# Optimization experiments

Measured on AMD Instinct MI355X. Metric: run time of the kernel, lower is better.

## Reference

```python
import jax, jax.numpy as jnp
import numpy as np

SR = 4  # search_range
D = 2 * SR + 1  # 9
NC = D * D      # 81 output channels


def setup_inputs() -> dict:
    key = jax.random.key(0)
    k1, k2 = jax.random.split(key)
    B, C, H, W = 8, 64, 192, 256
    x1 = jax.random.normal(k1, (B, C, H, W), dtype=jnp.float32)
    x2 = jax.random.normal(k2, (B, C, H, W), dtype=jnp.float32)
    return {"x1": x1, "x2": x2}


def reference(x1, x2):
    B, C, H, W = x1.shape
    # Zero-pad x2 so out-of-overlap products are zero, matching the
    # zero-initialized cv in the original module.
    x2p = jnp.pad(x2, ((0, 0), (0, 0), (SR, SR), (SR, SR)))
    outs = [None] * NC
    for i in range(-SR, SR + 1):
        for j in range(-SR, SR + 1):
            # Original torch code uses cv[:, 9*i + j] with negative wraparound.
            k = (D * i + j) % NC
            # x2 sample position is (h - i, w - j); in padded coords start = SR - i.
            shifted = jax.lax.dynamic_slice(
                x2p, (0, 0, SR - i, SR - j), (B, C, H, W))
            outs[k] = jnp.sum(x1 * shifted, axis=1)  # [B, H, W]
    cv = jnp.stack(outs, axis=1)  # [B, 81, H, W]
    return cv / NC
```

## Files before the change

### kernel.cpp

```cpp
#include <hip/hip_runtime.h>

#define HH 192
#define WW 256
#define CCH 4
#define NCHUNK 16
#define THREADS 512
#define CHSTEP (CCH * HH * WW)
#define ROWF 264
#define CHF  (8 * ROWF)
#define BUFF (CCH * CHF)
#define NSTRIPS 33

typedef float f4 __attribute__((ext_vector_type(4)));

#define GLL(gp, lp) __builtin_amdgcn_global_load_lds(                        \
    (const __attribute__((address_space(1))) unsigned int*)(gp),            \
    (__attribute__((address_space(3))) unsigned int*)(lp), 16, 0, 0)

__global__ __launch_bounds__(THREADS) void cost_volume_kernel(
    const float* __restrict__ x1, const float* __restrict__ x2,
    float* __restrict__ out)
{
    __shared__ __align__(16) float smem[2 * BUFF];

    const int tid  = threadIdx.x;
    const int wave = tid >> 6;
    const int lane = tid & 63;

    const int bid = blockIdx.x;
    const bool isB = (bid >= 1536);
    int b, hout, hbase, drow;
    if (!isB) {
        b     = bid & 7;
        hout  = bid >> 3;
        hbase = hout - 3;
        drow  = 7 - wave;
    } else {
        const int t = bid - 1536;
        b     = t & 7;
        const int h0 = (t >> 3) << 3;
        hout  = h0 + wave;
        hbase = h0 - 4;
        drow  = wave;
    }

    auto desc = [&](int s, int& goff) {
        const int u = (s << 6) + lane;
        const int ch = u / 528, v = u % 528;
        const int d = v / 66, cu = v % 66;
        const int hg = hbase + d, wg = (cu << 2) - 4;
        const bool ok = (cu >= 1) & (cu <= 64) & (hg >= 0) & (hg < HH);
        goff = ok ? (((b * 64 + ch) * HH + hg) * WW + wg) : -1;
    };
    int g0, g1, g2, g3, g4;
    desc(wave,      g0);
    desc(wave + 8,  g1);
    desc(wave + 16, g2);
    desc(wave + 24, g3);
    desc(32,        g4);
    if (wave != 0) g4 = -1;

    auto issue = [&](int nb, int n) {
        const int cofs = n * CHSTEP;
        float* const base = smem + nb * BUFF;
        if (g0 >= 0) GLL(x2 + g0 + cofs, base + (wave << 8));
        if (g1 >= 0) GLL(x2 + g1 + cofs, base + ((wave + 8) << 8));
        if (g2 >= 0) GLL(x2 + g2 + cofs, base + ((wave + 16) << 8));
        if (g3 >= 0) GLL(x2 + g3 + cofs, base + ((wave + 24) << 8));
        if (g4 >= 0) GLL(x2 + g4 + cofs, base + (32 << 8));
    };

    const f4 z4 = {0.f, 0.f, 0.f, 0.f};
    for (int z = tid; z < 2 * BUFF / 4; z += THREADS) ((f4*)smem)[z] = z4;
    __syncthreads();

    const float* x1base = x1 + ((b * 64) * HH + hout) * WW + (lane << 2);

    issue(0, 0);
    f4 aC0 = *(const f4*)(x1base);
    f4 aC1 = *(const f4*)(x1base + HH * WW);
    f4 aC2 = *(const f4*)(x1base + 2 * HH * WW);
    f4 aC3 = *(const f4*)(x1base + 3 * HH * WW);
    __syncthreads();

    f4 acc0 = z4, acc1 = z4, acc2 = z4, acc3 = z4, acc4 = z4,
       acc5 = z4, acc6 = z4, acc7 = z4, acc8 = z4;

    for (int n = 0; n < NCHUNK; ++n) {
        f4 aN0 = z4, aN1 = z4, aN2 = z4, aN3 = z4;
        if (n + 1 < NCHUNK) {
            issue((n + 1) & 1, n + 1);
            const float* x1c = x1base + (n + 1) * CHSTEP;
            aN0 = *(const f4*)(x1c);
            aN1 = *(const f4*)(x1c + HH * WW);
            aN2 = *(const f4*)(x1c + 2 * HH * WW);
            aN3 = *(const f4*)(x1c + 3 * HH * WW);
        }
        const float* sb2 = smem + (n & 1) * BUFF + drow * ROWF + (lane << 2);

#define CV_CC(CC, AV)                                                        \
        {                                                                    \
            const f4 xv0 = *(const f4*)(sb2 + (CC) * CHF);                   \
            const f4 xv1 = *(const f4*)(sb2 + (CC) * CHF + 4);               \
            const f4 xv2 = *(const f4*)(sb2 + (CC) * CHF + 8);               \
            const f4 w8 = xv0;                                               \
            const f4 w7 = __builtin_shufflevector(xv0, xv1, 1, 2, 3, 4);     \
            const f4 w6 = __builtin_shufflevector(xv0, xv1, 2, 3, 4, 5);     \
            const f4 w5 = __builtin_shufflevector(xv0, xv1, 3, 4, 5, 6);     \
            const f4 w4 = xv1;                                               \
            const f4 w3 = __builtin_shufflevector(xv1, xv2, 1, 2, 3, 4);     \
            const f4 w2 = __builtin_shufflevector(xv1, xv2, 2, 3, 4, 5);     \
            const f4 w1w = __builtin_shufflevector(xv1, xv2, 3, 4, 5, 6);    \
            const f4 w0w = xv2;                                              \
            acc0 = __builtin_elementwise_fma(AV, w0w, acc0);                 \
            acc1 = __builtin_elementwise_fma(AV, w1w, acc1);                 \
            acc2 = __builtin_elementwise_fma(AV, w2, acc2);                  \
            acc3 = __builtin_elementwise_fma(AV, w3, acc3);                  \
            acc4 = __builtin_elementwise_fma(AV, w4, acc4);                  \
            acc5 = __builtin_elementwise_fma(AV, w5, acc5);                  \
            acc6 = __builtin_elementwise_fma(AV, w6, acc6);                  \
            acc7 = __builtin_elementwise_fma(AV, w7, acc7);                  \
            acc8 = __builtin_elementwise_fma(AV, w8, acc8);                  \
        }
        CV_CC(0, aC0)
        CV_CC(1, aC1)
        CV_CC(2, aC2)
        CV_CC(3, aC3)
#undef CV_CC

        aC0 = aN0;
        aC1 = aN1;
        aC2 = aN2;
        aC3 = aN3;
        __syncthreads();
    }

    const float scale = 1.0f / 81.0f;
    const int wout = lane << 2;
#define CV_OUT(JJ)                                                           \
    {                                                                        \
        const int k = isB ? (32 + (JJ)) : (9 * wave + (JJ) + 41) % 81;       \
        float* po = out + (((long)b * 81 + k) * HH + hout) * WW + wout;      \
        *(f4*)po = acc##JJ * scale;                                          \
    }
    CV_OUT(0) CV_OUT(1) CV_OUT(2) CV_OUT(3) CV_OUT(4)
    CV_OUT(5) CV_OUT(6) CV_OUT(7) CV_OUT(8)
#undef CV_OUT
}

extern "C" void kernel_launch(void* const* d_in, const int* in_sizes, int n_in,
                              void* d_out, int out_size, void* d_ws, size_t ws_size,
                              hipStream_t stream) {
    const float* x1 = (const float*)d_in[0];
    const float* x2 = (const float*)d_in[1];
    float* out = (float*)d_out;
    dim3 grid(1536 + 192);
    dim3 block(THREADS);
    hipLaunchKernelGGL(cost_volume_kernel, grid, block, 0, stream, x1, x2, out);
}
```

Baseline: 119.3 us.

## Pack channel pairs into fp16 and accumulate with v_dot2_f32_f16

```diff
diff --git a/kernel.cpp b/kernel.cpp
--- a/kernel.cpp
+++ b/kernel.cpp
@@ -2,26 +2,39 @@
 
 #define HH 192
 #define WW 256
-#define CCH 4
+#define HW (HH * WW)
 #define NCHUNK 16
 #define THREADS 512
-#define CHSTEP (CCH * HH * WW)
-#define ROWF 264
-#define CHF  (8 * ROWF)
-#define BUFF (CCH * CHF)
-#define NSTRIPS 33
+#define CH4 (4 * HW)
+#define ROWD 264
+#define CPD (8 * ROWD)
+#define BUFD (2 * CPD)
+#define UPW 132
 
 typedef float f4 __attribute__((ext_vector_type(4)));
+typedef unsigned int u32;
+typedef u32 u4 __attribute__((ext_vector_type(4)));
+typedef _Float16 h2 __attribute__((ext_vector_type(2)));
 
-#define GLL(gp, lp) __builtin_amdgcn_global_load_lds(                        \
-    (const __attribute__((address_space(1))) unsigned int*)(gp),            \
-    (__attribute__((address_space(3))) unsigned int*)(lp), 16, 0, 0)
+static __device__ __forceinline__ float dot2f(u32 a, u32 b, float c) {
+#if __has_builtin(__builtin_amdgcn_fdot2)
+    return __builtin_amdgcn_fdot2(__builtin_bit_cast(h2, a),
+                                  __builtin_bit_cast(h2, b), c, false);
+#else
+    float d;
+    asm("v_dot2_f32_f16 %0, %1, %2, %3" : "=v"(d) : "v"(a), "v"(b), "v"(c));
+    return d;
+#endif
+}
+static __device__ __forceinline__ u32 pkh(float lo, float hi) {
+    return __builtin_bit_cast(u32, __builtin_amdgcn_cvt_pkrtz(lo, hi));
+}
 
 __global__ __launch_bounds__(THREADS) void cost_volume_kernel(
     const float* __restrict__ x1, const float* __restrict__ x2,
     float* __restrict__ out)
 {
-    __shared__ __align__(16) float smem[2 * BUFF];
+    __shared__ u32 smem[2 * BUFD];
 
     const int tid  = threadIdx.x;
     const int wave = tid >> 6;
@@ -29,111 +42,126 @@
 
     const int bid = blockIdx.x;
     const bool isB = (bid >= 1536);
-    int b, hout, hbase, drow;
+    int b, hout, rbase, drow;
     if (!isB) {
         b     = bid & 7;
         hout  = bid >> 3;
-        hbase = hout - 3;
+        rbase = hout - 3;
         drow  = 7 - wave;
     } else {
         const int t = bid - 1536;
         b     = t & 7;
         const int h0 = (t >> 3) << 3;
         hout  = h0 + wave;
-        hbase = h0 - 4;
+        rbase = h0 - 4;
         drow  = wave;
     }
 
-    auto desc = [&](int s, int& goff) {
-        const int u = (s << 6) + lane;
-        const int ch = u / 528, v = u % 528;
-        const int d = v / 66, cu = v % 66;
-        const int hg = hbase + d, wg = (cu << 2) - 4;
-        const bool ok = (cu >= 1) & (cu <= 64) & (hg >= 0) & (hg < HH);
-        goff = ok ? (((b * 64 + ch) * HH + hg) * WW + wg) : -1;
+    int g0, g1, g2, l0, l1, l2;
+    bool wr0, wr1, wr2;
+    auto mk = [&](int m, int& g, int& l, bool& wr) {
+        const int q = (m << 6) + lane;
+        const int u = wave * UPW + q;
+        const int cp = u / 528, v = u % 528;
+        const int row = v / 66, cu = v % 66;
+        const int hg = rbase + row;
+        wr = (q < UPW);
+        const bool okl = wr & (cu >= 1) & (cu <= 64) & (hg >= 0) & (hg < HH);
+        g = okl ? (((b * 64 + 2 * cp) * HH + hg) * WW + (cu << 2) - 4) : -1;
+        l = cp * CPD + row * ROWD + (cu << 2);
     };
-    int g0, g1, g2, g3, g4;
-    desc(wave,      g0);
-    desc(wave + 8,  g1);
-    desc(wave + 16, g2);
-    desc(wave + 24, g3);
-    desc(32,        g4);
-    if (wave != 0) g4 = -1;
+    mk(0, g0, l0, wr0);
+    mk(1, g1, l1, wr1);
+    mk(2, g2, l2, wr2);
 
-    auto issue = [&](int nb, int n) {
-        const int cofs = n * CHSTEP;
-        float* const base = smem + nb * BUFF;
-        if (g0 >= 0) GLL(x2 + g0 + cofs, base + (wave << 8));
-        if (g1 >= 0) GLL(x2 + g1 + cofs, base + ((wave + 8) << 8));
-        if (g2 >= 0) GLL(x2 + g2 + cofs, base + ((wave + 16) << 8));
-        if (g3 >= 0) GLL(x2 + g3 + cofs, base + ((wave + 24) << 8));
-        if (g4 >= 0) GLL(x2 + g4 + cofs, base + (32 << 8));
+    const f4 z4 = {0.f, 0.f, 0.f, 0.f};
+    f4 qa0 = z4, qb0 = z4, qa1 = z4, qb1 = z4, qa2 = z4, qb2 = z4;
+    auto issue_stage = [&](int n) {
+        const int o = n * CH4;
+        qa0 = (g0 >= 0) ? *(const f4*)(x2 + g0 + o)      : z4;
+        qb0 = (g0 >= 0) ? *(const f4*)(x2 + g0 + o + HW) : z4;
+        qa1 = (g1 >= 0) ? *(const f4*)(x2 + g1 + o)      : z4;
+        qb1 = (g1 >= 0) ? *(const f4*)(x2 + g1 + o + HW) : z4;
+        qa2 = (g2 >= 0) ? *(const f4*)(x2 + g2 + o)      : z4;
+        qb2 = (g2 >= 0) ? *(const f4*)(x2 + g2 + o + HW) : z4;
+    };
+    auto write_stage = [&](int nb) {
+        u32* bp = smem + nb * BUFD;
+        if (wr0) { u4 t = {pkh(qa0[0], qb0[0]), pkh(qa0[1], qb0[1]),
+                           pkh(qa0[2], qb0[2]), pkh(qa0[3], qb0[3])};
+                   *(u4*)(bp + l0) = t; }
+        if (wr1) { u4 t = {pkh(qa1[0], qb1[0]), pkh(qa1[1], qb1[1]),
+                           pkh(qa1[2], qb1[2]), pkh(qa1[3], qb1[3])};
+                   *(u4*)(bp + l1) = t; }
+        if (wr2) { u4 t = {pkh(qa2[0], qb2[0]), pkh(qa2[1], qb2[1]),
+                           pkh(qa2[2], qb2[2]), pkh(qa2[3], qb2[3])};
+                   *(u4*)(bp + l2) = t; }
     };
 
-    const f4 z4 = {0.f, 0.f, 0.f, 0.f};
-    for (int z = tid; z < 2 * BUFF / 4; z += THREADS) ((f4*)smem)[z] = z4;
-    __syncthreads();
+    const float* x1p = x1 + ((b * 64) * HH + hout) * WW + (lane << 2);
+    f4 r0, r1, r2, r3;
+    auto load_x1 = [&](int n) {
+        const float* p = x1p + n * CH4;
+        r0 = *(const f4*)p;
+        r1 = *(const f4*)(p + HW);
+        r2 = *(const f4*)(p + 2 * HW);
+        r3 = *(const f4*)(p + 3 * HW);
+    };
 
-    const float* x1base = x1 + ((b * 64) * HH + hout) * WW + (lane << 2);
-
-    issue(0, 0);
-    f4 aC0 = *(const f4*)(x1base);
-    f4 aC1 = *(const f4*)(x1base + HH * WW);
-    f4 aC2 = *(const f4*)(x1base + 2 * HH * WW);
-    f4 aC3 = *(const f4*)(x1base + 3 * HH * WW);
+    issue_stage(0);
+    load_x1(0);
+    write_stage(0);
     __syncthreads();
 
     f4 acc0 = z4, acc1 = z4, acc2 = z4, acc3 = z4, acc4 = z4,
        acc5 = z4, acc6 = z4, acc7 = z4, acc8 = z4;
 
+#define DJ(ACC, W, B0, B1, B2, B3)                                           \
+            ACC[0] = dot2f(W[0], B0, ACC[0]);                                \
+            ACC[1] = dot2f(W[1], B1, ACC[1]);                                \
+            ACC[2] = dot2f(W[2], B2, ACC[2]);                                \
+            ACC[3] = dot2f(W[3], B3, ACC[3]);
+#define CV(BP, A0, A1, A2, A3)                                               \
+        {                                                                    \
+            const u4 xv0 = *(const u4*)(BP);                                 \
+            const u4 xv1 = *(const u4*)((BP) + 4);                           \
+            const u4 xv2 = *(const u4*)((BP) + 8);                           \
+            const u4 w8v = xv0;                                              \
+            const u4 w7v = __builtin_shufflevector(xv0, xv1, 1, 2, 3, 4);    \
+            const u4 w6v = __builtin_shufflevector(xv0, xv1, 2, 3, 4, 5);    \
+            const u4 w5v = __builtin_shufflevector(xv0, xv1, 3, 4, 5, 6);    \
+            const u4 w4v = xv1;                                              \
+            const u4 w3v = __builtin_shufflevector(xv1, xv2, 1, 2, 3, 4);    \
+            const u4 w2v = __builtin_shufflevector(xv1, xv2, 2, 3, 4, 5);    \
+            const u4 w1v = __builtin_shufflevector(xv1, xv2, 3, 4, 5, 6);    \
+            const u4 w0v = xv2;                                              \
+            DJ(acc0, w0v, A0, A1, A2, A3)                                    \
+            DJ(acc1, w1v, A0, A1, A2, A3)                                    \
+            DJ(acc2, w2v, A0, A1, A2, A3)                                    \
+            DJ(acc3, w3v, A0, A1, A2, A3)                                    \
+            DJ(acc4, w4v, A0, A1, A2, A3)                                    \
+            DJ(acc5, w5v, A0, A1, A2, A3)                                    \
+            DJ(acc6, w6v, A0, A1, A2, A3)                                    \
+            DJ(acc7, w7v, A0, A1, A2, A3)                                    \
+            DJ(acc8, w8v, A0, A1, A2, A3)                                    \
+        }
+
     for (int n = 0; n < NCHUNK; ++n) {
-        f4 aN0 = z4, aN1 = z4, aN2 = z4, aN3 = z4;
-        if (n + 1 < NCHUNK) {
-            issue((n + 1) & 1, n + 1);
-            const float* x1c = x1base + (n + 1) * CHSTEP;
-            aN0 = *(const f4*)(x1c);
-            aN1 = *(const f4*)(x1c + HH * WW);
-            aN2 = *(const f4*)(x1c + 2 * HH * WW);
-            aN3 = *(const f4*)(x1c + 3 * HH * WW);
-        }
-        const float* sb2 = smem + (n & 1) * BUFF + drow * ROWF + (lane << 2);
+        const u32 pa0 = pkh(r0[0], r1[0]), pa1 = pkh(r0[1], r1[1]),
+                  pa2 = pkh(r0[2], r1[2]), pa3 = pkh(r0[3], r1[3]);
+        const u32 pb0 = pkh(r2[0], r3[0]), pb1 = pkh(r2[1], r3[1]),
+                  pb2 = pkh(r2[2], r3[2]), pb3 = pkh(r2[3], r3[3]);
+        if (n + 1 < NCHUNK) { issue_stage(n + 1); load_x1(n + 1); }
 
-#define CV_CC(CC, AV)                                                        \
-        {                                                                    \
-            const f4 xv0 = *(const f4*)(sb2 + (CC) * CHF);                   \
-            const f4 xv1 = *(const f4*)(sb2 + (CC) * CHF + 4);               \
-            const f4 xv2 = *(const f4*)(sb2 + (CC) * CHF + 8);               \
-            const f4 w8 = xv0;                                               \
-            const f4 w7 = __builtin_shufflevector(xv0, xv1, 1, 2, 3, 4);     \
-            const f4 w6 = __builtin_shufflevector(xv0, xv1, 2, 3, 4, 5);     \
-            const f4 w5 = __builtin_shufflevector(xv0, xv1, 3, 4, 5, 6);     \
-            const f4 w4 = xv1;                                               \
-            const f4 w3 = __builtin_shufflevector(xv1, xv2, 1, 2, 3, 4);     \
-            const f4 w2 = __builtin_shufflevector(xv1, xv2, 2, 3, 4, 5);     \
-            const f4 w1w = __builtin_shufflevector(xv1, xv2, 3, 4, 5, 6);    \
-            const f4 w0w = xv2;                                              \
-            acc0 = __builtin_elementwise_fma(AV, w0w, acc0);                 \
-            acc1 = __builtin_elementwise_fma(AV, w1w, acc1);                 \
-            acc2 = __builtin_elementwise_fma(AV, w2, acc2);                  \
-            acc3 = __builtin_elementwise_fma(AV, w3, acc3);                  \
-            acc4 = __builtin_elementwise_fma(AV, w4, acc4);                  \
-            acc5 = __builtin_elementwise_fma(AV, w5, acc5);                  \
-            acc6 = __builtin_elementwise_fma(AV, w6, acc6);                  \
-            acc7 = __builtin_elementwise_fma(AV, w7, acc7);                  \
-            acc8 = __builtin_elementwise_fma(AV, w8, acc8);                  \
-        }
-        CV_CC(0, aC0)
-        CV_CC(1, aC1)
-        CV_CC(2, aC2)
-        CV_CC(3, aC3)
-#undef CV_CC
+        const u32* base2 = smem + (n & 1) * BUFD + drow * ROWD + (lane << 2);
+        CV(base2,       pa0, pa1, pa2, pa3)
+        CV(base2 + CPD, pb0, pb1, pb2, pb3)
 
-        aC0 = aN0;
-        aC1 = aN1;
-        aC2 = aN2;
-        aC3 = aN3;
+        if (n + 1 < NCHUNK) write_stage((n + 1) & 1);
         __syncthreads();
     }
+#undef CV
+#undef DJ
 
     const float scale = 1.0f / 81.0f;
     const int wout = lane << 2;
```

Result: slower. 166.5 us (+39.6%).
